# Kernel optimization log

Hardware: AMD Instinct MI355X
Metric: run time of the kernel (lower is better)

Reference implementation:

```python
import jax
import jax.numpy as jnp
from jax import lax
import numpy as np

DIM = 1024
T = 2048
B = 16
N_GROUPS = 32
DELTA_INIT = -2.0


def _xavier(key, shape, gain=1.0):
    fan_in, fan_out = shape[1], shape[0]
    limit = gain * np.sqrt(6.0 / (fan_in + fan_out))
    return jax.random.uniform(key, shape, jnp.float32, -limit, limit)


def setup_inputs() -> dict:
    key = jax.random.key(0)
    k_x, k_wx, k_wd, k_wo = jax.random.split(key, 4)
    return {
        "x": jax.random.normal(k_x, (T, B, DIM), jnp.float32),
        "h0": jnp.zeros((B, DIM), jnp.float32),
        "W_x": _xavier(k_wx, (DIM, DIM)),
        "r_h": jnp.zeros((DIM,), jnp.float32),
        "b": jnp.zeros((DIM,), jnp.float32),
        "W_delta": _xavier(k_wd, (DIM, DIM), gain=0.1),
        "b_delta": jnp.full((DIM,), DELTA_INIT, jnp.float32),
        "W_out": _xavier(k_wo, (DIM, DIM)),
        "n_groups": N_GROUPS,
    }


def reference(x, h0, W_x, r_h, b, W_delta, b_delta, W_out, n_groups):
    Tn, Bn, D = x.shape
    gs = D // n_groups  # group_size
    # Precompute all input-dependent GEMMs in parallel over (T, B).
    delta = jax.nn.sigmoid(jnp.einsum('tbd,ed->tbe', x, W_delta) + b_delta)  # [T,B,D]
    cand_in = jnp.einsum('tbd,ed->tbe', x, W_x) + b                          # [T,B,D]

    def step(h_prev, inp):
        d_t, c_t = inp
        candidate = jnp.tanh(c_t + r_h * h_prev)           # diagonal recurrence
        h_new = (1.0 - d_t) * h_prev + d_t * candidate     # [B,D]
        compete = jax.nn.softmax(
            h_new.reshape(Bn, n_groups, gs), axis=-1).reshape(Bn, D)
        out = compete * jax.nn.silu(h_new @ W_out.T)
        return h_new, (h_new, out)

    _, (hs, outs) = lax.scan(step, h0, (delta, cand_in))
    h_all = jnp.concatenate([h0[None], hs], axis=0)  # [T+1,B,D]
    return h_all, outs
```

## Files before the change

### kernel.cpp

```cpp
#include <hip/hip_runtime.h>
#include <stdint.h>

#define DIMN 1024
#define TSTEPS 2048
#define BATCH 16
#define MTOT (TSTEPS*BATCH)
#define CH (BATCH*DIMN)

typedef unsigned short u16;
typedef __attribute__((ext_vector_type(8))) __bf16 bf16x8;
typedef __attribute__((ext_vector_type(4))) float floatx4;

__device__ __forceinline__ float bf2f(u16 u) {
    unsigned v = ((unsigned)u) << 16;
    return __builtin_bit_cast(float, v);
}
__device__ __forceinline__ u16 f2bf(float f) {
    __bf16 b = (__bf16)f;
    return __builtin_bit_cast(u16, b);
}
__device__ __forceinline__ void gl_lds16(const void* g, void* l) {
    __builtin_amdgcn_global_load_lds(
        (const __attribute__((address_space(1))) void*)g,
        (__attribute__((address_space(3))) void*)l,
        16, 0, 0);
}

#define LOG2E  1.4426950408889634f
#define LOG2E2 2.8853900817779268f

__global__ void cvt_kernel(const float* __restrict__ src, u16* __restrict__ dst, int n4) {
    int i = blockIdx.x * blockDim.x + threadIdx.x;
    if (i >= n4) return;
    float4 v = ((const float4*)src)[i];
    ushort4 o;
    o.x = f2bf(v.x); o.y = f2bf(v.y); o.z = f2bf(v.z); o.w = f2bf(v.w);
    ((ushort4*)dst)[i] = o;
}

__global__ __launch_bounds__(256) void gemm_bt(
    const u16* __restrict__ A, const u16* __restrict__ W,
    const float* __restrict__ bias,
    u16* __restrict__ outB, float* __restrict__ outF,
    const u16* __restrict__ cmp, int mode)
{
    __shared__ alignas(16) u16 a_sh[128 * 32];
    __shared__ alignas(16) u16 b_sh[128 * 32];
    const int tid  = threadIdx.x;
    const int lane = tid & 63;
    const int wave = tid >> 6;
    const int wm = wave & 1, wn = wave >> 1;
    const int m0 = blockIdx.x * 128, n0 = blockIdx.y * 128;
    const int row = lane & 15, quad = lane >> 4;

    const u16* Ag0 = A + (size_t)(m0 + (tid >> 2)) * DIMN + (tid & 3) * 8;
    const u16* Ag1 = Ag0 + (size_t)64 * DIMN;
    const u16* Wg0 = W + (size_t)(n0 + (tid >> 2)) * DIMN + (tid & 3) * 8;
    const u16* Wg1 = Wg0 + (size_t)64 * DIMN;
    u16* a_d0 = a_sh + tid * 8; u16* a_d1 = a_sh + 2048 + tid * 8;
    u16* b_d0 = b_sh + tid * 8; u16* b_d1 = b_sh + 2048 + tid * 8;

    floatx4 acc[4][4];
    #pragma unroll
    for (int i = 0; i < 4; i++)
        #pragma unroll
        for (int j = 0; j < 4; j++) acc[i][j] = (floatx4)(0.0f);

    int aoff[4], boff[4];
    #pragma unroll
    for (int i = 0; i < 4; i++) aoff[i] = (wm * 64 + i * 16 + row) * 32 + quad * 8;
    #pragma unroll
    for (int j = 0; j < 4; j++) boff[j] = (wn * 64 + j * 16 + row) * 32 + quad * 8;

    for (int kt = 0; kt < DIMN; kt += 32) {
        __syncthreads();
        gl_lds16(Ag0 + kt, a_d0);
        gl_lds16(Ag1 + kt, a_d1);
        gl_lds16(Wg0 + kt, b_d0);
        gl_lds16(Wg1 + kt, b_d1);
        __syncthreads();
        bf16x8 av[4], bv[4];
        #pragma unroll
        for (int i = 0; i < 4; i++) av[i] = *(const bf16x8*)(a_sh + aoff[i]);
        #pragma unroll
        for (int j = 0; j < 4; j++) bv[j] = *(const bf16x8*)(b_sh + boff[j]);
        #pragma unroll
        for (int i = 0; i < 4; i++)
            #pragma unroll
            for (int j = 0; j < 4; j++)
                acc[i][j] = __builtin_amdgcn_mfma_f32_16x16x32_bf16(av[i], bv[j], acc[i][j], 0, 0, 0);
    }

    const int mb = m0 + wm * 64 + quad * 4;
    const int nb = n0 + wn * 64 + row;
    if (mode == 2) {
        #pragma unroll
        for (int i = 0; i < 4; i++)
            #pragma unroll
            for (int j = 0; j < 4; j++)
                #pragma unroll
                for (int r = 0; r < 4; r++) {
                    size_t idx = (size_t)(mb + i * 16 + r) * DIMN + (nb + j * 16);
                    float z = acc[i][j][r];
                    float sil = z * __builtin_amdgcn_rcpf(1.f + __builtin_amdgcn_exp2f(-z * LOG2E));
                    outF[idx] = bf2f(cmp[idx]) * sil;
                }
    } else if (mode == 0) {
        #pragma unroll
        for (int i = 0; i < 4; i++)
            #pragma unroll
            for (int j = 0; j < 4; j++)
                #pragma unroll
                for (int r = 0; r < 4; r++) {
                    int n = nb + j * 16;
                    float v = acc[i][j][r] + bias[n];
                    v = __builtin_amdgcn_rcpf(1.f + __builtin_amdgcn_exp2f(-v * LOG2E));
                    outB[(size_t)(mb + i * 16 + r) * DIMN + n] = f2bf(v);
                }
    } else {
        #pragma unroll
        for (int i = 0; i < 4; i++)
            #pragma unroll
            for (int j = 0; j < 4; j++)
                #pragma unroll
                for (int r = 0; r < 4; r++) {
                    int n = nb + j * 16;
                    float v = acc[i][j][r] + bias[n];
                    outB[(size_t)(mb + i * 16 + r) * DIMN + n] = f2bf(v);
                }
    }
}

#define CS 64
#define SB 8
__global__ __launch_bounds__(64) void scan_kernel(
    const u16* __restrict__ dB, const u16* __restrict__ cB,
    const float* __restrict__ h0, const float* __restrict__ r_h,
    float* __restrict__ hAll, u16* __restrict__ hB)
{
    __shared__ alignas(16) u16 d_sh[2][CS * 64];
    __shared__ alignas(16) u16 c_sh[2][CS * 64];
    const int tid = threadIdx.x;
    const int c0 = blockIdx.x * 64;
    const int c  = c0 + tid;
    const int d  = c & (DIMN - 1);

    float h = h0[c];
    const float r2 = r_h[d] * LOG2E2;
    hAll[c] = h;

    const u16* dG = dB + (size_t)(tid >> 3) * CH + c0 + (tid & 7) * 8;
    const u16* cG = cB + (size_t)(tid >> 3) * CH + c0 + (tid & 7) * 8;

    #pragma unroll
    for (int s = 0; s < 8; s++) {
        gl_lds16(dG + (size_t)(s * 8) * CH, (void*)&d_sh[0][s * 512]);
        gl_lds16(cG + (size_t)(s * 8) * CH, (void*)&c_sh[0][s * 512]);
    }

    float* hOut = hAll + CH + c;
    u16* hbOut  = hB + c;

    for (int t0 = 0; t0 < TSTEPS; t0 += CS) {
        const int buf = (t0 / CS) & 1;
        if (t0 + CS < TSTEPS) {
            #pragma unroll
            for (int s = 0; s < 8; s++) {
                gl_lds16(dG + (size_t)(t0 + CS + s * 8) * CH, (void*)&d_sh[buf ^ 1][s * 512]);
                gl_lds16(cG + (size_t)(t0 + CS + s * 8) * CH, (void*)&c_sh[buf ^ 1][s * 512]);
            }
            asm volatile("s_waitcnt vmcnt(16)" ::: "memory");
        } else {
            asm volatile("s_waitcnt vmcnt(0)" ::: "memory");
        }
        __builtin_amdgcn_sched_barrier(0);

        const u16* dS = d_sh[buf];
        const u16* cS = c_sh[buf];

        #pragma unroll
        for (int sb = 0; sb < CS / SB; sb++) {
            #pragma unroll
            for (int i = 0; i < SB; i++) {
                const int s = sb * SB + i;
                float dlt  = bf2f(dS[s * 64 + tid]);
                float cin2 = bf2f(cS[s * 64 + tid]) * LOG2E2;
                float e    = __builtin_amdgcn_exp2f(fmaf(r2, h, cin2));
                float q    = __builtin_amdgcn_rcpf(e + 1.f);
                float base = fmaf(-dlt, h, h) + dlt;
                float m2d  = -2.f * dlt;
                h = fmaf(m2d, q, base);
                hOut[(size_t)(t0 + s) * CH] = h;
                hbOut[(size_t)(t0 + s) * CH] = f2bf(h);
            }
        }
    }
}

__global__ __launch_bounds__(256) void post_kernel(
    const float* __restrict__ hAll, u16* __restrict__ cmp)
{
    const int gid = blockIdx.x * 256 + threadIdx.x;
    float4 hv = ((const float4*)(hAll + CH))[gid];

    float ex = __builtin_amdgcn_exp2f(hv.x * LOG2E);
    float ey = __builtin_amdgcn_exp2f(hv.y * LOG2E);
    float ez = __builtin_amdgcn_exp2f(hv.z * LOG2E);
    float ew = __builtin_amdgcn_exp2f(hv.w * LOG2E);
    float sum = (ex + ey) + (ez + ew);
    #pragma unroll
    for (int s = 4; s > 0; s >>= 1) sum += __shfl_xor(sum, s);
    float inv = __builtin_amdgcn_rcpf(sum);

    ushort4 co;
    co.x = f2bf(ex * inv); co.y = f2bf(ey * inv);
    co.z = f2bf(ez * inv); co.w = f2bf(ew * inv);
    ((ushort4*)cmp)[gid] = co;
}

extern "C" void kernel_launch(void* const* d_in, const int* in_sizes, int n_in,
                              void* d_out, int out_size, void* d_ws, size_t ws_size,
                              hipStream_t stream) {
    const float* x   = (const float*)d_in[0];
    const float* h0  = (const float*)d_in[1];
    const float* W_x = (const float*)d_in[2];
    const float* r_h = (const float*)d_in[3];
    const float* b   = (const float*)d_in[4];
    const float* W_d = (const float*)d_in[5];
    const float* b_d = (const float*)d_in[6];
    const float* W_o = (const float*)d_in[7];
    float* out = (float*)d_out;

    char* ws = (char*)d_ws;
    u16* xb   = (u16*)(ws);
    u16* wdB  = (u16*)(ws + 67108864);
    u16* wxB  = (u16*)(ws + 69206016);
    u16* woB  = (u16*)(ws + 71303168);
    u16* dBuf = (u16*)(ws + 73400320);
    u16* cBuf = (u16*)(ws + 140509184);
    u16* cmpB = (u16*)(ws + 207618048);
    u16* hB   = xb;

    cvt_kernel<<<dim3(33554432 / 4 / 256), 256, 0, stream>>>(x, xb, 33554432 / 4);
    cvt_kernel<<<dim3(1048576 / 4 / 256), 256, 0, stream>>>(W_d, wdB, 1048576 / 4);
    cvt_kernel<<<dim3(1048576 / 4 / 256), 256, 0, stream>>>(W_x, wxB, 1048576 / 4);
    cvt_kernel<<<dim3(1048576 / 4 / 256), 256, 0, stream>>>(W_o, woB, 1048576 / 4);

    dim3 g(MTOT / 128, DIMN / 128);
    gemm_bt<<<g, 256, 0, stream>>>(xb, wdB, b_d, dBuf, nullptr, nullptr, 0);
    gemm_bt<<<g, 256, 0, stream>>>(xb, wxB, b,   cBuf, nullptr, nullptr, 1);
    scan_kernel<<<256, 64, 0, stream>>>(dBuf, cBuf, h0, r_h, out, hB);
    post_kernel<<<dim3(TSTEPS * CH / 4 / 256), 256, 0, stream>>>(out, cmpB);
    gemm_bt<<<g, 256, 0, stream>>>(hB, woB, nullptr, nullptr, out + 33570816, cmpB, 2);
}
```

Measured before the change: 865.5 us.

## Double-buffer GEMM LDS tiles, reorder block mapping, move bf16 h write to post kernel

The GEMM now uses two LDS buffers so global-to-LDS loads for the next K slice are issued before the MFMAs on the current slice run, replacing the two barriers per iteration with a prefetch/compute ping-pong. The grid is flattened so consecutive blocks share the same A row tile across the 8 N tiles, which should improve L2 reuse of A. The bf16 copy of h is no longer written inside the serial scan and is produced in the parallel post kernel instead, taking store traffic off the latency-bound scan at the cost of post_kernel writing one extra output. LDS use per block doubles, which may reduce occupancy.

```diff
diff --git a/kernel.cpp b/kernel.cpp
--- a/kernel.cpp
+++ b/kernel.cpp
@@ -44,21 +44,20 @@
     u16* __restrict__ outB, float* __restrict__ outF,
     const u16* __restrict__ cmp, int mode)
 {
-    __shared__ alignas(16) u16 a_sh[128 * 32];
-    __shared__ alignas(16) u16 b_sh[128 * 32];
+    __shared__ alignas(16) u16 a_sh[2][128 * 32];
+    __shared__ alignas(16) u16 b_sh[2][128 * 32];
     const int tid  = threadIdx.x;
     const int lane = tid & 63;
     const int wave = tid >> 6;
     const int wm = wave & 1, wn = wave >> 1;
-    const int m0 = blockIdx.x * 128, n0 = blockIdx.y * 128;
+    const int fid = blockIdx.x;
+    const int m0 = (fid >> 3) * 128, n0 = (fid & 7) * 128;
     const int row = lane & 15, quad = lane >> 4;
 
     const u16* Ag0 = A + (size_t)(m0 + (tid >> 2)) * DIMN + (tid & 3) * 8;
     const u16* Ag1 = Ag0 + (size_t)64 * DIMN;
     const u16* Wg0 = W + (size_t)(n0 + (tid >> 2)) * DIMN + (tid & 3) * 8;
     const u16* Wg1 = Wg0 + (size_t)64 * DIMN;
-    u16* a_d0 = a_sh + tid * 8; u16* a_d1 = a_sh + 2048 + tid * 8;
-    u16* b_d0 = b_sh + tid * 8; u16* b_d1 = b_sh + 2048 + tid * 8;
 
     floatx4 acc[4][4];
     #pragma unroll
@@ -72,24 +71,47 @@
     #pragma unroll
     for (int j = 0; j < 4; j++) boff[j] = (wn * 64 + j * 16 + row) * 32 + quad * 8;
 
-    for (int kt = 0; kt < DIMN; kt += 32) {
-        __syncthreads();
-        gl_lds16(Ag0 + kt, a_d0);
-        gl_lds16(Ag1 + kt, a_d1);
-        gl_lds16(Wg0 + kt, b_d0);
-        gl_lds16(Wg1 + kt, b_d1);
-        __syncthreads();
-        bf16x8 av[4], bv[4];
-        #pragma unroll
-        for (int i = 0; i < 4; i++) av[i] = *(const bf16x8*)(a_sh + aoff[i]);
-        #pragma unroll
-        for (int j = 0; j < 4; j++) bv[j] = *(const bf16x8*)(b_sh + boff[j]);
-        #pragma unroll
-        for (int i = 0; i < 4; i++)
-            #pragma unroll
-            for (int j = 0; j < 4; j++)
-                acc[i][j] = __builtin_amdgcn_mfma_f32_16x16x32_bf16(av[i], bv[j], acc[i][j], 0, 0, 0);
-    }
+    gl_lds16(Ag0, &a_sh[0][tid * 8]);
+    gl_lds16(Ag1, &a_sh[0][2048 + tid * 8]);
+    gl_lds16(Wg0, &b_sh[0][tid * 8]);
+    gl_lds16(Wg1, &b_sh[0][2048 + tid * 8]);
+    asm volatile("s_waitcnt vmcnt(0)" ::: "memory");
+    __builtin_amdgcn_s_barrier();
+
+    #define COMPUTE(b)                                                             \
+    {                                                                              \
+        bf16x8 av[4], bv[4];                                                       \
+        _Pragma("unroll")                                                          \
+        for (int i = 0; i < 4; i++) av[i] = *(const bf16x8*)(&a_sh[b][aoff[i]]);   \
+        _Pragma("unroll")                                                          \
+        for (int j = 0; j < 4; j++) bv[j] = *(const bf16x8*)(&b_sh[b][boff[j]]);   \
+        _Pragma("unroll")                                                          \
+        for (int i = 0; i < 4; i++)                                                \
+            _Pragma("unroll")                                                      \
+            for (int j = 0; j < 4; j++)                                            \
+                acc[i][j] = __builtin_amdgcn_mfma_f32_16x16x32_bf16(               \
+                    av[i], bv[j], acc[i][j], 0, 0, 0);                             \
+    }
+
+    for (int kt = 0; kt < DIMN; kt += 64) {
+        gl_lds16(Ag0 + kt + 32, &a_sh[1][tid * 8]);
+        gl_lds16(Ag1 + kt + 32, &a_sh[1][2048 + tid * 8]);
+        gl_lds16(Wg0 + kt + 32, &b_sh[1][tid * 8]);
+        gl_lds16(Wg1 + kt + 32, &b_sh[1][2048 + tid * 8]);
+        COMPUTE(0);
+        asm volatile("s_waitcnt vmcnt(0)" ::: "memory");
+        __builtin_amdgcn_s_barrier();
+        if (kt + 64 < DIMN) {
+            gl_lds16(Ag0 + kt + 64, &a_sh[0][tid * 8]);
+            gl_lds16(Ag1 + kt + 64, &a_sh[0][2048 + tid * 8]);
+            gl_lds16(Wg0 + kt + 64, &b_sh[0][tid * 8]);
+            gl_lds16(Wg1 + kt + 64, &b_sh[0][2048 + tid * 8]);
+        }
+        COMPUTE(1);
+        asm volatile("s_waitcnt vmcnt(0)" ::: "memory");
+        __builtin_amdgcn_s_barrier();
+    }
+    #undef COMPUTE
 
     const int mb = m0 + wm * 64 + quad * 4;
     const int nb = n0 + wn * 64 + row;
@@ -136,7 +158,7 @@
 __global__ __launch_bounds__(64) void scan_kernel(
     const u16* __restrict__ dB, const u16* __restrict__ cB,
     const float* __restrict__ h0, const float* __restrict__ r_h,
-    float* __restrict__ hAll, u16* __restrict__ hB)
+    float* __restrict__ hAll)
 {
     __shared__ alignas(16) u16 d_sh[2][CS * 64];
     __shared__ alignas(16) u16 c_sh[2][CS * 64];
@@ -159,7 +181,6 @@
     }
 
     float* hOut = hAll + CH + c;
-    u16* hbOut  = hB + c;
 
     for (int t0 = 0; t0 < TSTEPS; t0 += CS) {
         const int buf = (t0 / CS) & 1;
@@ -191,14 +212,13 @@
                 float m2d  = -2.f * dlt;
                 h = fmaf(m2d, q, base);
                 hOut[(size_t)(t0 + s) * CH] = h;
-                hbOut[(size_t)(t0 + s) * CH] = f2bf(h);
             }
         }
     }
 }
 
 __global__ __launch_bounds__(256) void post_kernel(
-    const float* __restrict__ hAll, u16* __restrict__ cmp)
+    const float* __restrict__ hAll, u16* __restrict__ hB, u16* __restrict__ cmp)
 {
     const int gid = blockIdx.x * 256 + threadIdx.x;
     float4 hv = ((const float4*)(hAll + CH))[gid];
@@ -212,10 +232,12 @@
     for (int s = 4; s > 0; s >>= 1) sum += __shfl_xor(sum, s);
     float inv = __builtin_amdgcn_rcpf(sum);
 
-    ushort4 co;
+    ushort4 co, ho;
     co.x = f2bf(ex * inv); co.y = f2bf(ey * inv);
     co.z = f2bf(ez * inv); co.w = f2bf(ew * inv);
+    ho.x = f2bf(hv.x); ho.y = f2bf(hv.y); ho.z = f2bf(hv.z); ho.w = f2bf(hv.w);
     ((ushort4*)cmp)[gid] = co;
+    ((ushort4*)hB)[gid] = ho;
 }
 
 extern "C" void kernel_launch(void* const* d_in, const int* in_sizes, int n_in,
@@ -246,10 +268,10 @@
     cvt_kernel<<<dim3(1048576 / 4 / 256), 256, 0, stream>>>(W_x, wxB, 1048576 / 4);
     cvt_kernel<<<dim3(1048576 / 4 / 256), 256, 0, stream>>>(W_o, woB, 1048576 / 4);
 
-    dim3 g(MTOT / 128, DIMN / 128);
+    dim3 g(MTOT / 128 * (DIMN / 128));
     gemm_bt<<<g, 256, 0, stream>>>(xb, wdB, b_d, dBuf, nullptr, nullptr, 0);
     gemm_bt<<<g, 256, 0, stream>>>(xb, wxB, b,   cBuf, nullptr, nullptr, 1);
-    scan_kernel<<<256, 64, 0, stream>>>(dBuf, cBuf, h0, r_h, out, hB);
-    post_kernel<<<dim3(TSTEPS * CH / 4 / 256), 256, 0, stream>>>(out, cmpB);
+    scan_kernel<<<256, 64, 0, stream>>>(dBuf, cBuf, h0, r_h, out);
+    post_kernel<<<dim3(TSTEPS * CH / 4 / 256), 256, 0, stream>>>(out, hB, cmpB);
     gemm_bt<<<g, 256, 0, stream>>>(hB, woB, nullptr, nullptr, out + 33570816, cmpB, 2);
 }
```

Measured after the change: 878.9 us. No clear change (+1.6%).

## Pipeline GEMM K-loop with 4-buffer LDS and move bf16 h conversion to post kernel

Applied to the files above, without the earlier changes.

The GEMM K-loop now uses a 4-deep LDS ring with loads issued two tiles ahead and vmcnt-based waits, so global-to-LDS copies overlap with MFMA work instead of sitting between two full barriers per step. The grid is flattened to 1D, and the tile index is decoded with M-fastest ordering. The scan kernel no longer writes a bf16 copy of h; the post kernel produces it while it already reads h. The scan's wait count is relaxed to vmcnt(63) after the first chunk so its serial loop stalls less on outstanding stores. This adds LDS use (64KB per block), which may lower occupancy, and the single barrier per iteration relies on the 4-buffer distance to avoid write-after-read hazards.

```diff
diff --git a/kernel.cpp b/kernel.cpp
--- a/kernel.cpp
+++ b/kernel.cpp
@@ -44,21 +44,20 @@
     u16* __restrict__ outB, float* __restrict__ outF,
     const u16* __restrict__ cmp, int mode)
 {
-    __shared__ alignas(16) u16 a_sh[128 * 32];
-    __shared__ alignas(16) u16 b_sh[128 * 32];
+    __shared__ alignas(16) u16 a_sh[4][128 * 32];
+    __shared__ alignas(16) u16 b_sh[4][128 * 32];
     const int tid  = threadIdx.x;
     const int lane = tid & 63;
     const int wave = tid >> 6;
     const int wm = wave & 1, wn = wave >> 1;
-    const int m0 = blockIdx.x * 128, n0 = blockIdx.y * 128;
+    const int fid = blockIdx.x;
+    const int m0 = (fid & 255) * 128, n0 = (fid >> 8) * 128;
     const int row = lane & 15, quad = lane >> 4;
 
     const u16* Ag0 = A + (size_t)(m0 + (tid >> 2)) * DIMN + (tid & 3) * 8;
     const u16* Ag1 = Ag0 + (size_t)64 * DIMN;
     const u16* Wg0 = W + (size_t)(n0 + (tid >> 2)) * DIMN + (tid & 3) * 8;
     const u16* Wg1 = Wg0 + (size_t)64 * DIMN;
-    u16* a_d0 = a_sh + tid * 8; u16* a_d1 = a_sh + 2048 + tid * 8;
-    u16* b_d0 = b_sh + tid * 8; u16* b_d1 = b_sh + 2048 + tid * 8;
 
     floatx4 acc[4][4];
     #pragma unroll
@@ -72,24 +71,39 @@
     #pragma unroll
     for (int j = 0; j < 4; j++) boff[j] = (wn * 64 + j * 16 + row) * 32 + quad * 8;
 
-    for (int kt = 0; kt < DIMN; kt += 32) {
-        __syncthreads();
-        gl_lds16(Ag0 + kt, a_d0);
-        gl_lds16(Ag1 + kt, a_d1);
-        gl_lds16(Wg0 + kt, b_d0);
-        gl_lds16(Wg1 + kt, b_d1);
-        __syncthreads();
+    #define STAGE(t_) {                                                        \
+        const int pb_ = (t_) & 3; const int kp_ = (t_) * 32;                   \
+        gl_lds16(Ag0 + kp_, &a_sh[pb_][tid * 8]);                              \
+        gl_lds16(Ag1 + kp_, &a_sh[pb_][2048 + tid * 8]);                       \
+        gl_lds16(Wg0 + kp_, &b_sh[pb_][tid * 8]);                              \
+        gl_lds16(Wg1 + kp_, &b_sh[pb_][2048 + tid * 8]);                       \
+    }
+
+    STAGE(0);
+    STAGE(1);
+
+    #pragma unroll
+    for (int t = 0; t < 32; t++) {
+        if (t + 2 < 32) STAGE(t + 2);
+        if (t < 30)        { asm volatile("s_waitcnt vmcnt(8)" ::: "memory"); }
+        else if (t == 30)  { asm volatile("s_waitcnt vmcnt(4)" ::: "memory"); }
+        else               { asm volatile("s_waitcnt vmcnt(0)" ::: "memory"); }
+        __builtin_amdgcn_sched_barrier(0);
+        __builtin_amdgcn_s_barrier();
+        const int buf = t & 3;
         bf16x8 av[4], bv[4];
         #pragma unroll
-        for (int i = 0; i < 4; i++) av[i] = *(const bf16x8*)(a_sh + aoff[i]);
-        #pragma unroll
-        for (int j = 0; j < 4; j++) bv[j] = *(const bf16x8*)(b_sh + boff[j]);
-        #pragma unroll
-        for (int i = 0; i < 4; i++)
-            #pragma unroll
-            for (int j = 0; j < 4; j++)
-                acc[i][j] = __builtin_amdgcn_mfma_f32_16x16x32_bf16(av[i], bv[j], acc[i][j], 0, 0, 0);
-    }
+        for (int i = 0; i < 4; i++) av[i] = *(const bf16x8*)(&a_sh[buf][aoff[i]]);
+        #pragma unroll
+        for (int j = 0; j < 4; j++) bv[j] = *(const bf16x8*)(&b_sh[buf][boff[j]]);
+        #pragma unroll
+        for (int i = 0; i < 4; i++)
+            #pragma unroll
+            for (int j = 0; j < 4; j++)
+                acc[i][j] = __builtin_amdgcn_mfma_f32_16x16x32_bf16(
+                    av[i], bv[j], acc[i][j], 0, 0, 0);
+    }
+    #undef STAGE
 
     const int mb = m0 + wm * 64 + quad * 4;
     const int nb = n0 + wn * 64 + row;
@@ -136,7 +150,7 @@
 __global__ __launch_bounds__(64) void scan_kernel(
     const u16* __restrict__ dB, const u16* __restrict__ cB,
     const float* __restrict__ h0, const float* __restrict__ r_h,
-    float* __restrict__ hAll, u16* __restrict__ hB)
+    float* __restrict__ hAll)
 {
     __shared__ alignas(16) u16 d_sh[2][CS * 64];
     __shared__ alignas(16) u16 c_sh[2][CS * 64];
@@ -159,7 +173,6 @@
     }
 
     float* hOut = hAll + CH + c;
-    u16* hbOut  = hB + c;
 
     for (int t0 = 0; t0 < TSTEPS; t0 += CS) {
         const int buf = (t0 / CS) & 1;
@@ -169,10 +182,9 @@
                 gl_lds16(dG + (size_t)(t0 + CS + s * 8) * CH, (void*)&d_sh[buf ^ 1][s * 512]);
                 gl_lds16(cG + (size_t)(t0 + CS + s * 8) * CH, (void*)&c_sh[buf ^ 1][s * 512]);
             }
-            asm volatile("s_waitcnt vmcnt(16)" ::: "memory");
-        } else {
-            asm volatile("s_waitcnt vmcnt(0)" ::: "memory");
         }
+        if (t0 == 0) { asm volatile("s_waitcnt vmcnt(16)" ::: "memory"); }
+        else         { asm volatile("s_waitcnt vmcnt(63)" ::: "memory"); }
         __builtin_amdgcn_sched_barrier(0);
 
         const u16* dS = d_sh[buf];
@@ -191,14 +203,13 @@
                 float m2d  = -2.f * dlt;
                 h = fmaf(m2d, q, base);
                 hOut[(size_t)(t0 + s) * CH] = h;
-                hbOut[(size_t)(t0 + s) * CH] = f2bf(h);
             }
         }
     }
 }
 
 __global__ __launch_bounds__(256) void post_kernel(
-    const float* __restrict__ hAll, u16* __restrict__ cmp)
+    const float* __restrict__ hAll, u16* __restrict__ hB, u16* __restrict__ cmp)
 {
     const int gid = blockIdx.x * 256 + threadIdx.x;
     float4 hv = ((const float4*)(hAll + CH))[gid];
@@ -212,10 +223,12 @@
     for (int s = 4; s > 0; s >>= 1) sum += __shfl_xor(sum, s);
     float inv = __builtin_amdgcn_rcpf(sum);
 
-    ushort4 co;
+    ushort4 co, ho;
     co.x = f2bf(ex * inv); co.y = f2bf(ey * inv);
     co.z = f2bf(ez * inv); co.w = f2bf(ew * inv);
+    ho.x = f2bf(hv.x); ho.y = f2bf(hv.y); ho.z = f2bf(hv.z); ho.w = f2bf(hv.w);
     ((ushort4*)cmp)[gid] = co;
+    ((ushort4*)hB)[gid] = ho;
 }
 
 extern "C" void kernel_launch(void* const* d_in, const int* in_sizes, int n_in,
@@ -246,10 +259,10 @@
     cvt_kernel<<<dim3(1048576 / 4 / 256), 256, 0, stream>>>(W_x, wxB, 1048576 / 4);
     cvt_kernel<<<dim3(1048576 / 4 / 256), 256, 0, stream>>>(W_o, woB, 1048576 / 4);
 
-    dim3 g(MTOT / 128, DIMN / 128);
+    dim3 g(MTOT / 128 * (DIMN / 128));
     gemm_bt<<<g, 256, 0, stream>>>(xb, wdB, b_d, dBuf, nullptr, nullptr, 0);
     gemm_bt<<<g, 256, 0, stream>>>(xb, wxB, b,   cBuf, nullptr, nullptr, 1);
-    scan_kernel<<<256, 64, 0, stream>>>(dBuf, cBuf, h0, r_h, out, hB);
-    post_kernel<<<dim3(TSTEPS * CH / 4 / 256), 256, 0, stream>>>(out, cmpB);
+    scan_kernel<<<256, 64, 0, stream>>>(dBuf, cBuf, h0, r_h, out);
+    post_kernel<<<dim3(TSTEPS * CH / 4 / 256), 256, 0, stream>>>(out, hB, cmpB);
     gemm_bt<<<g, 256, 0, stream>>>(hB, woB, nullptr, nullptr, out + 33570816, cmpB, 2);
 }
```

Result: faster. 808.7 us (-6.6%).
